# Kernel tuning notes

Hardware: AMD Instinct MI355X
Metric: run time of the kernel (lower is better)

Reference implementation:

```python
import math
import jax, jax.numpy as jnp
import numpy as np

TEMPERATURE = 1.0  # matches init kwarg

S, B, T, D = 16, 4, 1024, 2048


def setup_inputs() -> dict:
    key = jax.random.key(0)
    k1, k2 = jax.random.split(key)
    layer_query = jax.random.normal(k1, (D,), dtype=jnp.float32)
    source_bank = jax.random.normal(k2, (S, B, T, D), dtype=jnp.float32)
    return {"layer_query": layer_query, "source_bank": source_bank, "num_sources": S}


def reference(layer_query, source_bank, num_sources):
    # RMSNorm over last dim of the key bank (torch F.rms_norm with eps=None
    # uses the dtype's machine epsilon)
    eps = jnp.finfo(source_bank.dtype).eps
    ms = jnp.mean(jnp.square(source_bank), axis=-1, keepdims=True)  # [s,b,t,1]
    keys = source_bank * jax.lax.rsqrt(ms + eps)
    d = source_bank.shape[-1]
    scale = 1.0 / (math.sqrt(d) * TEMPERATURE)
    query = layer_query.astype(source_bank.dtype)
    scores = jnp.einsum('d,sbtd->sbt', query, keys) * scale  # [s,b,t]
    weights = jax.nn.softmax(scores, axis=0)                 # softmax over sources
    mixed = jnp.einsum('sbt,sbtd->btd', weights, source_bank)
    return mixed
```

## Files before the change

kernel.cpp:

```cpp
#include <hip/hip_runtime.h>
#include <stdint.h>


#define NSRC  16
#define NB    4
#define NT    1024
#define ND    2048
#define TILES 16
#define NBLK  256

typedef __fp16 half2_t __attribute__((ext_vector_type(2)));

__global__ __launch_bounds__(1024, 4)
void dar_persist_kernel(const float* __restrict__ q,
                        const float* __restrict__ bank,
                        float* __restrict__ out) {
    __shared__ __align__(16) uint32_t buf[2][NSRC][ND / 2];
    __shared__ float s_sc[2][NSRC];

    const int tid  = threadIdx.x;
    const int wave = tid >> 6;
    const int lane = tid & 63;
    const int bt0  = blockIdx.x * TILES;

    const float4* q4 = reinterpret_cast<const float4*>(q);
    float4 qr[8];
    #pragma unroll
    for (int i = 0; i < 8; ++i) qr[i] = q4[i * 64 + lane];

    const float4* srcbase = reinterpret_cast<const float4*>(bank)
                          + ((size_t)wave * (NB * NT) + bt0) * (ND / 4);

    float4 rA[8], rB[8];
    #pragma unroll
    for (int i = 0; i < 8; ++i) rA[i] = srcbase[i * 64 + lane];

    auto body = [&](int t, float4 (&cur)[8], float4 (&nxt)[8]) {
        const int c  = t & 1;
        const int bt = bt0 + t;

        float p2 = 0.0f, pq = 0.0f;
        #pragma unroll
        for (int i = 0; i < 8; ++i) {
            const float4 v = cur[i], qv = qr[i];
            p2 += v.x * v.x + v.y * v.y + v.z * v.z + v.w * v.w;
            pq += qv.x * v.x + qv.y * v.y + qv.z * v.z + qv.w * v.w;
        }
        #pragma unroll
        for (int m = 32; m >= 1; m >>= 1) {
            p2 += __shfl_xor(p2, m, 64);
            pq += __shfl_xor(pq, m, 64);
        }
        if (lane == 0) {
            const float ms = p2 * (1.0f / ND) + 1.1920928955078125e-07f;
            s_sc[c][wave]  = pq * rsqrtf(ms) * 0.022097086912079608f;
        }

        #pragma unroll
        for (int i = 0; i < 8; ++i) {
            const float4 v = cur[i];
            const half2_t lo = __builtin_amdgcn_cvt_pkrtz(v.x, v.y);
            const half2_t hi = __builtin_amdgcn_cvt_pkrtz(v.z, v.w);
            uint2 u;
            u.x = __builtin_bit_cast(uint32_t, lo);
            u.y = __builtin_bit_cast(uint32_t, hi);
            reinterpret_cast<uint2*>(&buf[c][wave][0])[i * 64 + lane] = u;
        }

        __syncthreads();

        if (t + 1 < TILES) {
            const float4* s2 = srcbase + (size_t)(t + 1) * (ND / 4);
            #pragma unroll
            for (int i = 0; i < 8; ++i) nxt[i] = s2[i * 64 + lane];
        }

        float w[NSRC], mx = -1e30f;
        #pragma unroll
        for (int s = 0; s < NSRC; ++s) { w[s] = s_sc[c][s]; mx = fmaxf(mx, w[s]); }
        float sum = 0.0f;
        #pragma unroll
        for (int s = 0; s < NSRC; ++s) { w[s] = __expf(w[s] - mx); sum += w[s]; }
        const float inv = 1.0f / sum;

        float ax = 0.0f, ay = 0.0f;
        #pragma unroll
        for (int s = 0; s < NSRC; ++s) {
            const half2_t h = __builtin_bit_cast(half2_t, buf[c][s][tid]);
            ax += w[s] * (float)h.x;
            ay += w[s] * (float)h.y;
        }
        float2 r;
        r.x = ax * inv;
        r.y = ay * inv;
        reinterpret_cast<float2*>(out + (size_t)bt * ND)[tid] = r;
    };

    for (int tt = 0; tt < TILES; tt += 2) {
        body(tt,     rA, rB);
        body(tt + 1, rB, rA);
    }
}

extern "C" void kernel_launch(void* const* d_in, const int* in_sizes, int n_in,
                              void* d_out, int out_size, void* d_ws, size_t ws_size,
                              hipStream_t stream) {
    const float* q    = (const float*)d_in[0];
    const float* bank = (const float*)d_in[1];
    float* out        = (float*)d_out;

    dim3 grid(NBLK);
    dim3 block(1024);
    dar_persist_kernel<<<grid, block, 0, stream>>>(q, bank, out);
}
```

Baseline: 122.4 us.

## Single-buffer LDS with raw barriers, drop register double-buffer, double grid size

The double-buffered LDS staging and the two register sets are replaced by one LDS buffer and a single register set. Two raw s_barriers per tile guard the reuse of that buffer, and the query is reloaded from global memory each tile instead of being held in registers. The grid grows to 512 blocks of 8 tiles each, and launch bounds ask for higher occupancy. The aim is lower LDS and register pressure so more blocks can be resident, at the cost of an extra barrier per tile, repeated query loads, and less overlap from the removed prefetch buffer.

Result: slower. 236.5 us (+93.2%).

```diff
diff --git a/kernel.cpp b/kernel.cpp
--- a/kernel.cpp
+++ b/kernel.cpp
@@ -6,99 +6,92 @@
 #define NB    4
 #define NT    1024
 #define ND    2048
-#define TILES 16
-#define NBLK  256
+#define TILES 8
+#define NBLK  512
 
-typedef __fp16 half2_t __attribute__((ext_vector_type(2)));
+typedef __fp16 h16x2 __attribute__((ext_vector_type(2)));
+typedef float  f32x4 __attribute__((ext_vector_type(4)));
 
-__global__ __launch_bounds__(1024, 4)
-void dar_persist_kernel(const float* __restrict__ q,
-                        const float* __restrict__ bank,
-                        float* __restrict__ out) {
-    __shared__ __align__(16) uint32_t buf[2][NSRC][ND / 2];
-    __shared__ float s_sc[2][NSRC];
+__global__ __launch_bounds__(1024, 8)
+void dar_pipe_kernel(const float* __restrict__ q,
+                     const float* __restrict__ bank,
+                     float* __restrict__ out) {
+    __shared__ uint32_t buf[NSRC][ND / 2];
+    __shared__ float s_sc[NSRC];
 
     const int tid  = threadIdx.x;
     const int wave = tid >> 6;
     const int lane = tid & 63;
     const int bt0  = blockIdx.x * TILES;
 
-    const float4* q4 = reinterpret_cast<const float4*>(q);
-    float4 qr[8];
+    const f32x4* srcbase = reinterpret_cast<const f32x4*>(bank)
+                         + ((size_t)wave * (NB * NT) + bt0) * (ND / 4);
+    const f32x4* q4 = reinterpret_cast<const f32x4*>(q);
+
+    f32x4 v[8];
     #pragma unroll
-    for (int i = 0; i < 8; ++i) qr[i] = q4[i * 64 + lane];
+    for (int i = 0; i < 8; ++i) v[i] = srcbase[i * 64 + lane];
 
-    const float4* srcbase = reinterpret_cast<const float4*>(bank)
-                          + ((size_t)wave * (NB * NT) + bt0) * (ND / 4);
-
-    float4 rA[8], rB[8];
-    #pragma unroll
-    for (int i = 0; i < 8; ++i) rA[i] = srcbase[i * 64 + lane];
-
-    auto body = [&](int t, float4 (&cur)[8], float4 (&nxt)[8]) {
-        const int c  = t & 1;
-        const int bt = bt0 + t;
-
+    for (int t = 0; t < TILES; ++t) {
         float p2 = 0.0f, pq = 0.0f;
         #pragma unroll
         for (int i = 0; i < 8; ++i) {
-            const float4 v = cur[i], qv = qr[i];
-            p2 += v.x * v.x + v.y * v.y + v.z * v.z + v.w * v.w;
-            pq += qv.x * v.x + qv.y * v.y + qv.z * v.z + qv.w * v.w;
+            const f32x4 qv = q4[i * 64 + lane];
+            const f32x4 x  = v[i];
+            p2 += x.x * x.x + x.y * x.y + x.z * x.z + x.w * x.w;
+            pq += qv.x * x.x + qv.y * x.y + qv.z * x.z + qv.w * x.w;
         }
         #pragma unroll
         for (int m = 32; m >= 1; m >>= 1) {
             p2 += __shfl_xor(p2, m, 64);
             pq += __shfl_xor(pq, m, 64);
         }
-        if (lane == 0) {
-            const float ms = p2 * (1.0f / ND) + 1.1920928955078125e-07f;
-            s_sc[c][wave]  = pq * rsqrtf(ms) * 0.022097086912079608f;
-        }
+
+        __builtin_amdgcn_s_barrier();
 
         #pragma unroll
         for (int i = 0; i < 8; ++i) {
-            const float4 v = cur[i];
-            const half2_t lo = __builtin_amdgcn_cvt_pkrtz(v.x, v.y);
-            const half2_t hi = __builtin_amdgcn_cvt_pkrtz(v.z, v.w);
+            const h16x2 lo = __builtin_amdgcn_cvt_pkrtz(v[i].x, v[i].y);
+            const h16x2 hi = __builtin_amdgcn_cvt_pkrtz(v[i].z, v[i].w);
             uint2 u;
             u.x = __builtin_bit_cast(uint32_t, lo);
             u.y = __builtin_bit_cast(uint32_t, hi);
-            reinterpret_cast<uint2*>(&buf[c][wave][0])[i * 64 + lane] = u;
+            reinterpret_cast<uint2*>(&buf[wave][0])[i * 64 + lane] = u;
+        }
+        if (lane == 0) {
+            s_sc[wave] = pq * rsqrtf(p2 * (1.0f / ND) + 1.1920928955078125e-07f)
+                       * 0.022097086912079608f;
+        }
+        asm volatile("s_waitcnt lgkmcnt(0)" ::: "memory");
+        __builtin_amdgcn_s_barrier();
+
+        if (t + 1 < TILES) {
+            const f32x4* s2 = srcbase + (size_t)(t + 1) * (ND / 4);
+            #pragma unroll
+            for (int i = 0; i < 8; ++i) v[i] = s2[i * 64 + lane];
         }
 
-        __syncthreads();
-
-        if (t + 1 < TILES) {
-            const float4* s2 = srcbase + (size_t)(t + 1) * (ND / 4);
-            #pragma unroll
-            for (int i = 0; i < 8; ++i) nxt[i] = s2[i * 64 + lane];
-        }
-
-        float w[NSRC], mx = -1e30f;
+        float sc[NSRC];
+        float mx = -1e30f;
         #pragma unroll
-        for (int s = 0; s < NSRC; ++s) { w[s] = s_sc[c][s]; mx = fmaxf(mx, w[s]); }
+        for (int s = 0; s < NSRC; ++s) { sc[s] = s_sc[s]; mx = fmaxf(mx, sc[s]); }
         float sum = 0.0f;
         #pragma unroll
-        for (int s = 0; s < NSRC; ++s) { w[s] = __expf(w[s] - mx); sum += w[s]; }
+        for (int s = 0; s < NSRC; ++s) { sc[s] = __expf(sc[s] - mx); sum += sc[s]; }
         const float inv = 1.0f / sum;
 
         float ax = 0.0f, ay = 0.0f;
         #pragma unroll
         for (int s = 0; s < NSRC; ++s) {
-            const half2_t h = __builtin_bit_cast(half2_t, buf[c][s][tid]);
-            ax += w[s] * (float)h.x;
-            ay += w[s] * (float)h.y;
+            const h16x2 h = __builtin_bit_cast(h16x2, buf[s][tid]);
+            const float w = sc[s] * inv;
+            ax += w * (float)h.x;
+            ay += w * (float)h.y;
         }
         float2 r;
-        r.x = ax * inv;
-        r.y = ay * inv;
-        reinterpret_cast<float2*>(out + (size_t)bt * ND)[tid] = r;
-    };
-
-    for (int tt = 0; tt < TILES; tt += 2) {
-        body(tt,     rA, rB);
-        body(tt + 1, rB, rA);
+        r.x = ax;
+        r.y = ay;
+        reinterpret_cast<float2*>(out + (size_t)(bt0 + t) * ND)[tid] = r;
     }
 }
 
@@ -111,5 +104,5 @@
 
     dim3 grid(NBLK);
     dim3 block(1024);
-    dar_persist_kernel<<<grid, block, 0, stream>>>(q, bank, out);
+    dar_pipe_kernel<<<grid, block, 0, stream>>>(q, bank, out);
 }
```
